# Optimization experiments

Hardware: AMD Instinct MI355X
Metric: run time of the kernel (lower is better)

The kernel has to match this reference:

```python
import jax, jax.numpy as jnp
import numpy as np

METRIC = (1.0, 1.0, 1.0, 1.0, -1.0)  # Cl(4,1) signature
N_HEADS = 8
EPS = 1e-6


def _cayley():
    # Cayley table C[a, b, k]: e_a * e_b = sum_k C[a,b,k] e_k, blades indexed by bitmask over 5 generators.
    C = np.zeros((32, 32, 32), dtype=np.float32)
    for a in range(32):
        for b in range(32):
            s = 0
            t = a >> 1
            while t:
                s += bin(t & b).count('1')
                t >>= 1
            sign = -1.0 if (s & 1) else 1.0
            for i in range(5):
                if (a & b) >> i & 1:
                    sign *= METRIC[i]
            C[a, b, a ^ b] = sign
    return C

_C_NP = _cayley()
GP_MAP = jnp.asarray(_C_NP)  # (32,32,32)
SIG = jnp.asarray(_C_NP[np.arange(32), np.arange(32), 0])  # blade square signs, (32,)


def normalize_cl41(x):
    # normalize each multivector (last-dim 32 blades) to unit RMS
    return x / jnp.sqrt(jnp.mean(x * x, axis=-1, keepdims=True) + EPS)


def versor_linear(x, W):
    # x: (B,S,I,32), W: (O,I,32); out_k = sum_{i,j,l} W[o,i,j] C[j,l,k] x[b,s,i,l]
    O, I, _ = W.shape
    W_op = jnp.einsum('oij,jlk->oilk', W, GP_MAP)  # (O,I,32,32)
    W_mat = W_op.transpose(1, 2, 0, 3).reshape(I * 32, O * 32)
    B, S = x.shape[0], x.shape[1]
    out = (x.reshape(B, S, I * 32) @ W_mat).reshape(B, S, O, 32)
    return normalize_cl41(out)


def versor_attention(x, Wq, Wk, Wv, Wo, lam):
    B, S, D, _ = x.shape
    H = N_HEADS
    hd = D // H

    def split_heads(t):  # (B,S,D,32) -> (B,H,S,hd,32)
        return t.reshape(B, S, H, hd, 32).transpose(0, 2, 1, 3, 4)

    q = split_heads(versor_linear(x, Wq))
    k = split_heads(versor_linear(x, Wk))
    v = split_heads(versor_linear(x, Wv))

    q_flat = (q * SIG).reshape(B, H, S, hd * 32)  # signature-weighted
    k_flat = k.reshape(B, H, S, hd * 32)

    scalar = jnp.einsum('bhsd,bhtd->bhst', q_flat, k_flat)
    scale = 1.0 / jnp.sqrt(jnp.asarray(hd, x.dtype))
    score = scalar * scale

    # torque term: sqrt(relu(|q|^2 |k|^2 - (q.k)^2) + eps) / sqrt(hd)
    q_norm_sq = jnp.sum(q_flat * q_flat, axis=-1)[..., :, None]  # (B,H,S,1)
    k_norm_sq = jnp.sum(k_flat * k_flat, axis=-1)[..., None, :]  # (B,H,1,S)
    torque = jnp.sqrt(jax.nn.relu(q_norm_sq * k_norm_sq - scalar * scalar) + EPS) * scale
    score = score + lam * torque

    probs = jax.nn.softmax(score, axis=-1)
    out = jnp.einsum('bhst,bhtdl->bhsdl', probs, v)  # (B,H,S,hd,32)
    out = out.transpose(0, 2, 1, 3, 4).reshape(B, S, D, 32)
    return versor_linear(out, Wo)


def setup_inputs() -> dict:
    key = jax.random.key(0)
    ks = jax.random.split(key, 5)
    B, S, D = 2, 1024, 128
    std = (2.0 / (D * 32)) ** 0.5  # Versor init
    x = jax.random.normal(ks[0], (B, S, D, 32), jnp.float32)
    Wq = jax.random.normal(ks[1], (D, D, 32), jnp.float32) * std
    Wk = jax.random.normal(ks[2], (D, D, 32), jnp.float32) * std
    Wv = jax.random.normal(ks[3], (D, D, 32), jnp.float32) * std
    Wo = jax.random.normal(ks[4], (D, D, 32), jnp.float32) * std
    attn_lambda = jnp.float32(0.1)
    return {'x': x, 'Wq': Wq, 'Wk': Wk, 'Wv': Wv, 'Wo': Wo, 'attn_lambda': attn_lambda}


def reference(x, Wq, Wk, Wv, Wo, attn_lambda):
    return versor_attention(x, Wq, Wk, Wv, Wo, attn_lambda)
```

## Files before the change

### kernel.cpp

```cpp
#include <hip/hip_runtime.h>
#include <stdint.h>

typedef __attribute__((ext_vector_type(4))) float    f32x4;
typedef __attribute__((ext_vector_type(8))) short    s16x8;
typedef __attribute__((ext_vector_type(4))) short    s16x4;
typedef __attribute__((ext_vector_type(8))) _Float16 f16x8;

#define DEV __device__ __forceinline__

DEV float blade_sign(int a, int b){
    int s = 0, t = a >> 1;
    while (t){ s += __popc(t & b); t >>= 1; }
    float sg = (s & 1) ? -1.0f : 1.0f;
    return ((a & b) & 16) ? -sg : sg;
}
DEV short f2h(float v){
    _Float16 h = (_Float16)v;
    return __builtin_bit_cast(short, h);
}
DEV float h2f(short b){
    return (float)__builtin_bit_cast(_Float16, b);
}
DEV void wait_vm(int n){
    if (n == 8)      asm volatile("s_waitcnt vmcnt(8)" ::: "memory");
    else if (n == 4) asm volatile("s_waitcnt vmcnt(4)" ::: "memory");
    else             asm volatile("s_waitcnt vmcnt(0)" ::: "memory");
}

__global__ __launch_bounds__(256) void cast_f32_f16(const float* __restrict__ in,
                                                    short* __restrict__ out){
    const size_t idx = (size_t)blockIdx.x * 256 + threadIdx.x;
    const float4* p = reinterpret_cast<const float4*>(in) + idx * 2;
    float4 a = p[0], b = p[1];
    s16x8 o;
    o[0]=f2h(a.x); o[1]=f2h(a.y); o[2]=f2h(a.z); o[3]=f2h(a.w);
    o[4]=f2h(b.x); o[5]=f2h(b.y); o[6]=f2h(b.z); o[7]=f2h(b.w);
    *reinterpret_cast<s16x8*>(out + idx * 8) = o;
}

DEV void build_wmat_body(const float* __restrict__ W, short* __restrict__ WmT,
                         int idx){
    const int n  = idx >> 9;
    const int kg = idx & 511;
    const int o = n >> 5, kb = n & 31;
    const int i = kg >> 2, l0 = (kg & 3) * 8;
    const float* wrow = W + (size_t)(o * 128 + i) * 32;
    s16x8 v;
    #pragma unroll
    for (int e = 0; e < 8; ++e){
        const int l = l0 + e, j = kb ^ l;
        v[e] = f2h(wrow[j] * blade_sign(j, l));
    }
    *reinterpret_cast<s16x8*>(WmT + (size_t)n * 4096 + kg * 8) = v;
}

__global__ __launch_bounds__(256) void build_wmat(const float* __restrict__ W,
                                                  short* __restrict__ WmT){
    build_wmat_body(W, WmT, blockIdx.x * 256 + threadIdx.x);
}

__global__ __launch_bounds__(256) void build_wmat3(const float* __restrict__ Wq,
                                                   const float* __restrict__ Wk,
                                                   const float* __restrict__ Wv,
                                                   short* __restrict__ WmT3){
    const int w = blockIdx.y;
    const float* W = (w == 0) ? Wq : ((w == 1) ? Wk : Wv);
    build_wmat_body(W, WmT3 + (size_t)w * 4096 * 4096,
                    blockIdx.x * 256 + threadIdx.x);
}

__global__ __launch_bounds__(256) void row_norms(const short* __restrict__ Q,
                                                 const short* __restrict__ Kq,
                                                 float* __restrict__ Nq,
                                                 float* __restrict__ Nk){
    const int row  = blockIdx.x * 4 + (threadIdx.x >> 6);
    const int lane = threadIdx.x & 63;
    const int b = row >> 13, h = (row >> 10) & 7, s = row & 1023;
    const size_t off = ((size_t)(b * 1024 + s)) * 4096 + h * 512 + lane * 8;
    s16x8 a = *reinterpret_cast<const s16x8*>(Q + off);
    s16x8 c = *reinterpret_cast<const s16x8*>(Kq + off);
    float sq = 0.f, sk = 0.f;
    #pragma unroll
    for (int e = 0; e < 8; ++e){
        float fa = h2f(a[e]); sq = fmaf(fa, fa, sq);
        float fc = h2f(c[e]); sk = fmaf(fc, fc, sk);
    }
    #pragma unroll
    for (int m = 1; m < 64; m <<= 1){
        sq += __shfl_xor(sq, m);
        sk += __shfl_xor(sk, m);
    }
    if (lane == 0){ Nq[row] = sq; Nk[row] = sk; }
}

__global__ __launch_bounds__(256) void softmax_rows(float* __restrict__ Sc){
    const int row  = blockIdx.x * 4 + (threadIdx.x >> 6);
    const int lane = threadIdx.x & 63;
    float* p = Sc + (size_t)row * 1024;
    float v[16];
    float mx = -3.0e38f;
    #pragma unroll
    for (int j = 0; j < 16; ++j){ v[j] = p[lane + j * 64]; mx = fmaxf(mx, v[j]); }
    #pragma unroll
    for (int m = 1; m < 64; m <<= 1) mx = fmaxf(mx, __shfl_xor(mx, m));
    float sum = 0.f;
    #pragma unroll
    for (int j = 0; j < 16; ++j){ v[j] = __expf(v[j] - mx); sum += v[j]; }
    #pragma unroll
    for (int m = 1; m < 64; m <<= 1) sum += __shfl_xor(sum, m);
    const float inv = 1.0f / sum;
    short* pb = reinterpret_cast<short*>(p);
    #pragma unroll
    for (int j = 0; j < 16; ++j) pb[lane + j * 64] = f2h(v[j] * inv);
}

#define GLOAD_LDS(gp, lp) \
    __builtin_amdgcn_global_load_lds( \
        (const __attribute__((address_space(1))) void*)(const void*)(gp), \
        (__attribute__((address_space(3))) void*)(void*)(lp), 16, 0, 0)

#define R3_TILE(T, WN, PF)                                                      \
  {                                                                             \
    const int bb = cur * 8192;                                                  \
    wait_vm(WN);                                                                \
    __builtin_amdgcn_s_barrier();                                               \
    asm volatile("" ::: "memory");                                              \
    __builtin_amdgcn_sched_barrier(0);                                          \
    const int sb = stg * 8192;                                                  \
    if (PF){                                                                    \
        GLOAD_LDS(gA0 + (size_t)((T) + 2) * 32, lds + sb + dA0);                \
        GLOAD_LDS(gA1 + (size_t)((T) + 2) * 32, lds + sb + dA1);                \
    }                                                                           \
    f16x8 av[4], bv[4];                                                         \
    _Pragma("unroll")                                                           \
    for (int i = 0; i < 4; ++i)                                                 \
        av[i] = *reinterpret_cast<const f16x8*>(lds + bb + ard + i * 512);      \
    bv[0] = *reinterpret_cast<const f16x8*>(lds + bb + brd + 0 * 512);          \
    bv[1] = *reinterpret_cast<const f16x8*>(lds + bb + brd + 1 * 512);          \
    __builtin_amdgcn_s_setprio(1);                                              \
    _Pragma("unroll")                                                           \
    for (int mi = 0; mi < 4; ++mi)                                              \
        _Pragma("unroll")                                                       \
        for (int ni = 0; ni < 2; ++ni)                                          \
            acc[mi][ni] = __builtin_amdgcn_mfma_f32_16x16x32_f16(               \
                av[mi], bv[ni], acc[mi][ni], 0, 0, 0);                          \
    __builtin_amdgcn_s_setprio(0);                                              \
    if (PF){                                                                    \
        GLOAD_LDS(gB0 + (size_t)((T) + 2) * 32, lds + sb + dB0);                \
        GLOAD_LDS(gB1 + (size_t)((T) + 2) * 32, lds + sb + dB1);                \
    }                                                                           \
    bv[2] = *reinterpret_cast<const f16x8*>(lds + bb + brd + 2 * 512);          \
    bv[3] = *reinterpret_cast<const f16x8*>(lds + bb + brd + 3 * 512);          \
    __builtin_amdgcn_s_setprio(1);                                              \
    _Pragma("unroll")                                                           \
    for (int mi = 0; mi < 4; ++mi)                                              \
        _Pragma("unroll")                                                       \
        for (int ni = 2; ni < 4; ++ni)                                          \
            acc[mi][ni] = __builtin_amdgcn_mfma_f32_16x16x32_f16(               \
                av[mi], bv[ni], acc[mi][ni], 0, 0, 0);                          \
    __builtin_amdgcn_s_setprio(0);                                              \
    cur = (cur == 2) ? 0 : cur + 1;                                             \
    stg = (stg == 2) ? 0 : stg + 1;                                             \
  }

template<int EPI, int CPX>
__global__ __launch_bounds__(256, 3) void versor_gemm_r3(
    const short* __restrict__ Abase, int lda,
    const short* __restrict__ Bbase, int ldb,
    int K, void* __restrict__ OutP,
    short* __restrict__ OQ, short* __restrict__ OK, short* __restrict__ OV)
{
    __shared__ short lds[3 * 8192];

    const int tid  = threadIdx.x;
    const int lane = tid & 63;
    const int wid  = tid >> 6;
    const int wr   = wid >> 1;
    const int wc   = wid & 1;
    const int z    = blockIdx.z;

    int bn, bm;
    if constexpr (CPX > 0){
        const int wg  = blockIdx.x + blockIdx.y * gridDim.x;
        const int xcd = wg & 7;
        const int u   = wg >> 3;
        bm = u & 15;
        bn = xcd * CPX + (u >> 4);
    } else {
        bn = blockIdx.x; bm = blockIdx.y;
    }

    const short* A = Abase;
    const short* B = Bbase;
    if constexpr (EPI == 5){
        A += (size_t)z * 1024 * 2048;
        B += (size_t)z * 512 * 1024;
    }
    const int row0 = bm * 128;
    const int col0 = bn * 128;

    const int jsw = ((lane & 3) ^ ((lane >> 3) & 3)) * 8;
    const short* gA0 = A + (size_t)(row0 + wid * 16 + (lane >> 2)) * lda + jsw;
    const short* gA1 = gA0 + (size_t)64 * lda;
    const short* gB0 = B + (size_t)(col0 + wid * 16 + (lane >> 2)) * ldb + jsw;
    const short* gB1 = gB0 + (size_t)64 * ldb;
    const int dA0 = wid * 512,        dA1 = 2048 + wid * 512;
    const int dB0 = 4096 + wid * 512, dB1 = 6144 + wid * 512;

    const int swz = ((lane >> 4) ^ (((lane & 15) >> 1) & 3)) * 8;
    const int ard = (wr * 64 + (lane & 15)) * 32 + swz;
    const int brd = 4096 + (wc * 64 + (lane & 15)) * 32 + swz;

    f32x4 acc[4][4];
    #pragma unroll
    for (int i = 0; i < 4; ++i)
        #pragma unroll
        for (int j = 0; j < 4; ++j)
            acc[i][j] = (f32x4){0.f, 0.f, 0.f, 0.f};

    const int NT = K >> 5;

    #pragma unroll
    for (int pt = 0; pt < 2; ++pt){
        const int sb = pt * 8192;
        GLOAD_LDS(gA0 + pt * 32, lds + sb + dA0);
        GLOAD_LDS(gA1 + pt * 32, lds + sb + dA1);
        GLOAD_LDS(gB0 + pt * 32, lds + sb + dB0);
        GLOAD_LDS(gB1 + pt * 32, lds + sb + dB1);
    }

    int cur = 0, stg = 2;
    for (int t = 0; t < NT - 1; ++t)
        R3_TILE(t, 4, (t + 2 < NT))
    R3_TILE(NT - 1, 0, false)

    const int rb = row0 + wr * 64 + (lane >> 4) * 4;
    const int cb = col0 + wc * 64 + (lane & 15);

    if constexpr (EPI == 0 || EPI == 3){
        #pragma unroll
        for (int mi = 0; mi < 4; ++mi){
            #pragma unroll
            for (int g = 0; g < 2; ++g){
                f32x4 a0 = acc[mi][2 * g], a1 = acc[mi][2 * g + 1];
                f32x4 ss = a0 * a0 + a1 * a1;
                #pragma unroll
                for (int m = 1; m < 16; m <<= 1){
                    ss.x += __shfl_xor(ss.x, m);
                    ss.y += __shfl_xor(ss.y, m);
                    ss.z += __shfl_xor(ss.z, m);
                    ss.w += __shfl_xor(ss.w, m);
                }
                f32x4 inv;
                inv.x = 1.0f / sqrtf(ss.x * 0.03125f + 1e-6f);
                inv.y = 1.0f / sqrtf(ss.y * 0.03125f + 1e-6f);
                inv.z = 1.0f / sqrtf(ss.z * 0.03125f + 1e-6f);
                inv.w = 1.0f / sqrtf(ss.w * 0.03125f + 1e-6f);
                acc[mi][2 * g]     = a0 * inv;
                acc[mi][2 * g + 1] = a1 * inv;
            }
        }
    }

    if constexpr (EPI == 0){
        const int zsel = col0 >> 12;
        const int cbm  = (col0 & 4095) + wc * 64 + (lane & 15);
        if (zsel == 0){
            const float sg0 = blade_sign(lane & 15, lane & 15);
            const float sg1 = blade_sign(16 | (lane & 15), 16 | (lane & 15));
            #pragma unroll
            for (int mi = 0; mi < 4; ++mi)
                #pragma unroll
                for (int ni = 0; ni < 4; ++ni){
                    const f32x4 v = acc[mi][ni] * ((ni & 1) ? sg1 : sg0);
                    #pragma unroll
                    for (int j = 0; j < 4; ++j)
                        OQ[(size_t)(rb + mi * 16 + j) * 4096 + (cbm + ni * 16)] = f2h(v[j]);
                }
        } else if (zsel == 1){
            #pragma unroll
            for (int mi = 0; mi < 4; ++mi)
                #pragma unroll
                for (int ni = 0; ni < 4; ++ni)
                    #pragma unroll
                    for (int j = 0; j < 4; ++j)
                        OK[(size_t)(rb + mi * 16 + j) * 4096 + (cbm + ni * 16)] = f2h(acc[mi][ni][j]);
        } else {
            #pragma unroll
            for (int mi = 0; mi < 4; ++mi){
                const int r = rb + mi * 16;
                const int b = r >> 10, tt = r & 1023;
                #pragma unroll
                for (int ni = 0; ni < 4; ++ni){
                    const int c = cbm + ni * 16;
                    const int h = c >> 9, f = c & 511;
                    s16x4 pv;
                    #pragma unroll
                    for (int j = 0; j < 4; ++j) pv[j] = f2h(acc[mi][ni][j]);
                    *reinterpret_cast<s16x4*>(OV + ((size_t)((b * 8 + h) * 512 + f)) * 1024 + tt) = pv;
                }
            }
        }
    }
    if constexpr (EPI == 3){
        float* Of = (float*)OutP;
        #pragma unroll
        for (int mi = 0; mi < 4; ++mi)
            #pragma unroll
            for (int ni = 0; ni < 4; ++ni)
                #pragma unroll
                for (int j = 0; j < 4; ++j)
                    Of[(size_t)(rb + mi * 16 + j) * 4096 + (cb + ni * 16)] = acc[mi][ni][j];
    }
    if constexpr (EPI == 5){
        short* Ob = (short*)OutP;
        const int b = z >> 3, h = z & 7;
        #pragma unroll
        for (int mi = 0; mi < 4; ++mi)
            #pragma unroll
            for (int ni = 0; ni < 4; ++ni)
                #pragma unroll
                for (int j = 0; j < 4; ++j)
                    Ob[(size_t)(b * 1024 + rb + mi * 16 + j) * 4096 + h * 512 + (cb + ni * 16)]
                        = f2h(acc[mi][ni][j]);
    }
}

#define SC_TILE(T, WN, PF)                                                      \
  {                                                                             \
    const int bb = ((T) & 3) * 16384;                                           \
    wait_vm(WN);                                                                \
    __builtin_amdgcn_s_barrier();                                               \
    asm volatile("" ::: "memory");                                              \
    __builtin_amdgcn_sched_barrier(0);                                          \
    if (PF){                                                                    \
        const int nb = (((T) + 3) & 3) * 16384;                                 \
        GLOAD_LDS(gA0 + (size_t)((T) + 3) * 32, lds + nb + dA0);                \
        GLOAD_LDS(gA1 + (size_t)((T) + 3) * 32, lds + nb + dA1);                \
    }                                                                           \
    f16x8 av[4], bv[4];                                                         \
    _Pragma("unroll")                                                           \
    for (int i = 0; i < 4; ++i){                                                \
        av[i] = *reinterpret_cast<const f16x8*>(lds + bb + ard + i * 512);      \
        bv[i] = *reinterpret_cast<const f16x8*>(lds + bb + brd + i * 512);      \
    }                                                                           \
    __builtin_amdgcn_s_setprio(1);                                              \
    _Pragma("unroll")                                                           \
    for (int mi = 0; mi < 4; ++mi)                                              \
        _Pragma("unroll")                                                       \
        for (int ni = 0; ni < 4; ++ni)                                          \
            acc[mi][ni] = __builtin_amdgcn_mfma_f32_16x16x32_f16(               \
                av[mi], bv[ni], acc[mi][ni], 0, 0, 0);                          \
    __builtin_amdgcn_s_setprio(0);                                              \
    if (PF){                                                                    \
        const int nb = (((T) + 3) & 3) * 16384;                                 \
        GLOAD_LDS(gB0 + (size_t)((T) + 3) * 32, lds + nb + dB0);                \
        GLOAD_LDS(gB1 + (size_t)((T) + 3) * 32, lds + nb + dB1);                \
    }                                                                           \
    f16x8 aw[4];                                                                \
    _Pragma("unroll")                                                           \
    for (int i = 0; i < 4; ++i)                                                 \
        aw[i] = *reinterpret_cast<const f16x8*>(lds + bb + ard + (4 + i) * 512);\
    __builtin_amdgcn_s_setprio(1);                                              \
    _Pragma("unroll")                                                           \
    for (int mi = 0; mi < 4; ++mi)                                              \
        _Pragma("unroll")                                                       \
        for (int ni = 0; ni < 4; ++ni)                                          \
            acc[4 + mi][ni] = __builtin_amdgcn_mfma_f32_16x16x32_f16(           \
                aw[mi], bv[ni], acc[4 + mi][ni], 0, 0, 0);                      \
    __builtin_amdgcn_s_setprio(0);                                              \
  }

__global__ __launch_bounds__(512, 2) void versor_gemm_sc(
    const short* __restrict__ Qbase, const short* __restrict__ Kbase,
    int K, float* __restrict__ OutP,
    const float* __restrict__ NqP, const float* __restrict__ NkP,
    const float* __restrict__ LamP)
{
    extern __shared__ short lds[];

    const int tid  = threadIdx.x;
    const int lane = tid & 63;
    const int wid  = tid >> 6;
    const int wm   = wid >> 2;
    const int wn   = wid & 3;
    const int z    = blockIdx.z;

    const int b = z >> 3, h = z & 7;
    const size_t off = (size_t)b * 1024 * 4096 + (size_t)h * 512;
    const short* A = Qbase + off;
    const short* B = Kbase + off;
    const int lda = 4096, ldb = 4096;
    const int row0 = blockIdx.y * 256;
    const int col0 = blockIdx.x * 256;

    const int jsw = ((lane & 3) ^ ((lane >> 3) & 3)) * 8;
    const short* gA0 = A + (size_t)(row0 + wid * 32 + (lane >> 2)) * lda + jsw;
    const short* gA1 = gA0 + (size_t)16 * lda;
    const short* gB0 = B + (size_t)(col0 + wid * 32 + (lane >> 2)) * ldb + jsw;
    const short* gB1 = gB0 + (size_t)16 * ldb;
    const int dA0 = wid * 1024, dA1 = dA0 + 512;
    const int dB0 = 8192 + wid * 1024, dB1 = dB0 + 512;

    const int swz = ((lane >> 4) ^ (((lane & 15) >> 1) & 3)) * 8;
    const int ard = (wm * 128 + (lane & 15)) * 32 + swz;
    const int brd = 8192 + (wn * 64 + (lane & 15)) * 32 + swz;

    f32x4 acc[8][4];
    #pragma unroll
    for (int i = 0; i < 8; ++i)
        #pragma unroll
        for (int j = 0; j < 4; ++j)
            acc[i][j] = (f32x4){0.f, 0.f, 0.f, 0.f};

    const int NT = K >> 5;

    #pragma unroll
    for (int pt = 0; pt < 3; ++pt){
        const int bb = pt * 16384;
        GLOAD_LDS(gA0 + pt * 32, lds + bb + dA0);
        GLOAD_LDS(gA1 + pt * 32, lds + bb + dA1);
        GLOAD_LDS(gB0 + pt * 32, lds + bb + dB0);
        GLOAD_LDS(gB1 + pt * 32, lds + bb + dB1);
    }

    for (int t = 0; t < NT - 2; ++t)
        SC_TILE(t, 8, (t + 3 < NT))
    SC_TILE(NT - 2, 4, false)
    SC_TILE(NT - 1, 0, false)

    const int rb = row0 + wm * 128 + (lane >> 4) * 4;
    const int cb = col0 + wn * 64 + (lane & 15);

    float* Of = OutP + (size_t)z * 1024 * 1024;
    const float lam = *LamP;
    const float* nq = NqP + z * 1024;
    const float* nk = NkP + z * 1024;
    #pragma unroll
    for (int mi = 0; mi < 8; ++mi)
        #pragma unroll
        for (int j = 0; j < 4; ++j){
            const int r = rb + mi * 16 + j;
            const float qn = nq[r];
            #pragma unroll
            for (int ni = 0; ni < 4; ++ni){
                const int c = cb + ni * 16;
                const float sc = acc[mi][ni][j];
                const float tq = sqrtf(fmaxf(qn * nk[c] - sc * sc, 0.0f) + 1e-6f);
                Of[(size_t)r * 1024 + c] = 0.25f * (sc + lam * tq);
            }
        }
}

extern "C" void kernel_launch(void* const* d_in, const int* in_sizes, int n_in,
                              void* d_out, int out_size, void* d_ws, size_t ws_size,
                              hipStream_t stream)
{
    (void)in_sizes; (void)n_in; (void)out_size; (void)ws_size;
    const float* x   = (const float*)d_in[0];
    const float* Wq  = (const float*)d_in[1];
    const float* Wk  = (const float*)d_in[2];
    const float* Wv  = (const float*)d_in[3];
    const float* Wo  = (const float*)d_in[4];
    const float* lam = (const float*)d_in[5];
    float* out = (float*)d_out;
    char*  ws  = (char*)d_ws;

    short* Xf   = (short*)(ws);
    short* WmT3 = (short*)(ws + (16u  << 20));
    short* Qf   = (short*)(ws + (112u << 20));
    short* Kf   = (short*)(ws + (128u << 20));
    short* Vt   = (short*)(ws + (144u << 20));
    float* Nq   = (float*)(ws + (160u << 20));
    float* Nk   = (float*)(ws + (160u << 20) + (64u << 10));
    float* Sc   = (float*)(ws + (16u  << 20));
    short* WmTo = (short*)(ws + (80u  << 20));
    short* Attn = Xf;

    const int DYN_LDS = 131072;
    hipFuncSetAttribute(reinterpret_cast<const void*>(versor_gemm_sc),
                        hipFuncAttributeMaxDynamicSharedMemorySize, DYN_LDS);

    dim3 blk(256), blk8(512);
    cast_f32_f16<<<4096, blk, 0, stream>>>(x, Xf);

    dim3 gw3(8192, 3);
    build_wmat3<<<gw3, blk, 0, stream>>>(Wq, Wk, Wv, WmT3);

    dim3 gqkv(96, 16, 1);
    versor_gemm_r3<0, 12><<<gqkv, blk, 0, stream>>>(
        Xf, 4096, WmT3, 4096, 4096, nullptr, Qf, Kf, Vt);

    row_norms<<<4096, blk, 0, stream>>>(Qf, Kf, Nq, Nk);

    build_wmat<<<8192, blk, 0, stream>>>(Wo, WmTo);

    dim3 gsc(4, 4, 16);
    versor_gemm_sc<<<gsc, blk8, DYN_LDS, stream>>>(Qf, Kf, 512, Sc, Nq, Nk, lam);
    softmax_rows<<<4096, blk, 0, stream>>>(Sc);

    dim3 gpv(4, 8, 16);
    versor_gemm_r3<5, 0><<<gpv, blk, 0, stream>>>(
        (const short*)Sc, 2048, Vt, 1024, 1024, Attn, nullptr, nullptr, nullptr);

    dim3 gfin(32, 16, 1);
    versor_gemm_r3<3, 4><<<gfin, blk, 0, stream>>>(
        Attn, 4096, WmTo, 4096, 4096, out, nullptr, nullptr, nullptr);
}
```

Measured before the change: 551.4 us.

## Add dedicated 256x128-tile QKV GEMM kernel with split prefetch scheduling

Replaces the generic r3 GEMM used for the fused QKV projection with a specialized kernel using 256x128 block tiles (each wave computing 128x64), a 3-stage LDS ring buffer, and B-tile prefetches interleaved between the two MFMA halves. The larger tile raises arithmetic intensity per LDS/global load and halves the grid. The normalization and Q/K/V scatter epilogue moves into the new kernel. The cost is more accumulator registers (128 floats) and 72KB LDS, which may limit occupancy to about 2 blocks per CU.

```diff
diff --git a/kernel.cpp b/kernel.cpp
--- a/kernel.cpp
+++ b/kernel.cpp
@@ -22,7 +22,9 @@
     return (float)__builtin_bit_cast(_Float16, b);
 }
 DEV void wait_vm(int n){
-    if (n == 8)      asm volatile("s_waitcnt vmcnt(8)" ::: "memory");
+    if (n == 12)     asm volatile("s_waitcnt vmcnt(12)" ::: "memory");
+    else if (n == 8) asm volatile("s_waitcnt vmcnt(8)" ::: "memory");
+    else if (n == 6) asm volatile("s_waitcnt vmcnt(6)" ::: "memory");
     else if (n == 4) asm volatile("s_waitcnt vmcnt(4)" ::: "memory");
     else             asm volatile("s_waitcnt vmcnt(0)" ::: "memory");
 }
@@ -119,6 +121,183 @@
         (const __attribute__((address_space(1))) void*)(const void*)(gp), \
         (__attribute__((address_space(3))) void*)(void*)(lp), 16, 0, 0)
 
+#define QKV_TILE(T, WN, PF)                                                     \
+  {                                                                             \
+    const int bb = cur * 12288;                                                 \
+    wait_vm(WN);                                                                \
+    __builtin_amdgcn_s_barrier();                                               \
+    asm volatile("" ::: "memory");                                              \
+    __builtin_amdgcn_sched_barrier(0);                                          \
+    const int sb = stg * 12288;                                                 \
+    if (PF){                                                                    \
+        GLOAD_LDS(gA0 + (size_t)((T) + 2) * 32, lds + sb + dA + 0 * 512);       \
+        GLOAD_LDS(gA1 + (size_t)((T) + 2) * 32, lds + sb + dA + 1 * 512);       \
+        GLOAD_LDS(gA2 + (size_t)((T) + 2) * 32, lds + sb + dA + 2 * 512);       \
+        GLOAD_LDS(gA3 + (size_t)((T) + 2) * 32, lds + sb + dA + 3 * 512);       \
+    }                                                                           \
+    f16x8 av[4], bv[4];                                                         \
+    _Pragma("unroll")                                                           \
+    for (int i = 0; i < 4; ++i){                                                \
+        av[i] = *reinterpret_cast<const f16x8*>(lds + bb + ard + i * 512);      \
+        bv[i] = *reinterpret_cast<const f16x8*>(lds + bb + brd + i * 512);      \
+    }                                                                           \
+    __builtin_amdgcn_s_setprio(1);                                              \
+    _Pragma("unroll")                                                           \
+    for (int mi = 0; mi < 4; ++mi)                                              \
+        _Pragma("unroll")                                                       \
+        for (int ni = 0; ni < 4; ++ni)                                          \
+            acc[mi][ni] = __builtin_amdgcn_mfma_f32_16x16x32_f16(               \
+                av[mi], bv[ni], acc[mi][ni], 0, 0, 0);                          \
+    __builtin_amdgcn_s_setprio(0);                                              \
+    if (PF){                                                                    \
+        GLOAD_LDS(gB0 + (size_t)((T) + 2) * 32, lds + sb + dB + 0 * 512);       \
+        GLOAD_LDS(gB1 + (size_t)((T) + 2) * 32, lds + sb + dB + 1 * 512);       \
+    }                                                                           \
+    f16x8 aw[4];                                                                \
+    _Pragma("unroll")                                                           \
+    for (int i = 0; i < 4; ++i)                                                 \
+        aw[i] = *reinterpret_cast<const f16x8*>(lds + bb + ard + (4 + i) * 512);\
+    __builtin_amdgcn_s_setprio(1);                                              \
+    _Pragma("unroll")                                                           \
+    for (int mi = 0; mi < 4; ++mi)                                              \
+        _Pragma("unroll")                                                       \
+        for (int ni = 0; ni < 4; ++ni)                                          \
+            acc[4 + mi][ni] = __builtin_amdgcn_mfma_f32_16x16x32_f16(           \
+                aw[mi], bv[ni], acc[4 + mi][ni], 0, 0, 0);                      \
+    __builtin_amdgcn_s_setprio(0);                                              \
+    cur = (cur == 2) ? 0 : cur + 1;                                             \
+    stg = (stg == 2) ? 0 : stg + 1;                                             \
+  }
+
+__global__ __launch_bounds__(256, 2) void versor_gemm_qkv2(
+    const short* __restrict__ Xf,
+    const short* __restrict__ WmT3,
+    short* __restrict__ OQ,
+    short* __restrict__ OK,
+    short* __restrict__ OV)
+{
+    extern __shared__ short lds[];
+
+    const int tid  = threadIdx.x;
+    const int lane = tid & 63;
+    const int wid  = tid >> 6;
+    const int wm   = wid >> 1;
+    const int wn   = wid & 1;
+
+    const int wg  = blockIdx.x + blockIdx.y * 96;
+    const int xcd = wg & 7;
+    const int u   = wg >> 3;
+    const int bm  = u & 7;
+    const int bn  = xcd * 12 + (u >> 3);
+    const int row0 = bm * 256;
+    const int col0 = bn * 128;
+
+    const int lda = 4096, ldb = 4096;
+
+    const int jsw = ((lane & 3) ^ ((lane >> 3) & 3)) * 8;
+    const short* gA0 = Xf + (size_t)(row0 + wid * 64 + (lane >> 2)) * lda + jsw;
+    const short* gA1 = gA0 + (size_t)16 * lda;
+    const short* gA2 = gA0 + (size_t)32 * lda;
+    const short* gA3 = gA0 + (size_t)48 * lda;
+    const short* gB0 = WmT3 + (size_t)(col0 + wid * 32 + (lane >> 2)) * ldb + jsw;
+    const short* gB1 = gB0 + (size_t)16 * ldb;
+    const int dA = wid * 4 * 512;
+    const int dB = 8192 + wid * 2 * 512;
+
+    const int swz = ((lane >> 4) ^ (((lane & 15) >> 1) & 3)) * 8;
+    const int ard = (wm * 128 + (lane & 15)) * 32 + swz;
+    const int brd = 8192 + (wn * 64 + (lane & 15)) * 32 + swz;
+
+    f32x4 acc[8][4];
+    #pragma unroll
+    for (int i = 0; i < 8; ++i)
+        #pragma unroll
+        for (int j = 0; j < 4; ++j)
+            acc[i][j] = (f32x4){0.f, 0.f, 0.f, 0.f};
+
+    const int NT = 4096 >> 5;
+
+    #pragma unroll
+    for (int pt = 0; pt < 2; ++pt){
+        const int sb = pt * 12288;
+        GLOAD_LDS(gA0 + pt * 32, lds + sb + dA + 0 * 512);
+        GLOAD_LDS(gA1 + pt * 32, lds + sb + dA + 1 * 512);
+        GLOAD_LDS(gA2 + pt * 32, lds + sb + dA + 2 * 512);
+        GLOAD_LDS(gA3 + pt * 32, lds + sb + dA + 3 * 512);
+        GLOAD_LDS(gB0 + pt * 32, lds + sb + dB + 0 * 512);
+        GLOAD_LDS(gB1 + pt * 32, lds + sb + dB + 1 * 512);
+    }
+
+    int cur = 0, stg = 2;
+    for (int t = 0; t < NT - 1; ++t)
+        QKV_TILE(t, 6, (t + 2 < NT))
+    QKV_TILE(NT - 1, 0, false)
+
+    const int rb = row0 + wm * 128 + (lane >> 4) * 4;
+
+    #pragma unroll
+    for (int mi = 0; mi < 8; ++mi){
+        #pragma unroll
+        for (int g = 0; g < 2; ++g){
+            f32x4 a0 = acc[mi][2 * g], a1 = acc[mi][2 * g + 1];
+            f32x4 ss = a0 * a0 + a1 * a1;
+            #pragma unroll
+            for (int m = 1; m < 16; m <<= 1){
+                ss.x += __shfl_xor(ss.x, m);
+                ss.y += __shfl_xor(ss.y, m);
+                ss.z += __shfl_xor(ss.z, m);
+                ss.w += __shfl_xor(ss.w, m);
+            }
+            f32x4 inv;
+            inv.x = 1.0f / sqrtf(ss.x * 0.03125f + 1e-6f);
+            inv.y = 1.0f / sqrtf(ss.y * 0.03125f + 1e-6f);
+            inv.z = 1.0f / sqrtf(ss.z * 0.03125f + 1e-6f);
+            inv.w = 1.0f / sqrtf(ss.w * 0.03125f + 1e-6f);
+            acc[mi][2 * g]     = a0 * inv;
+            acc[mi][2 * g + 1] = a1 * inv;
+        }
+    }
+
+    const int zsel = col0 >> 12;
+    const int cbm  = (col0 & 4095) + wn * 64 + (lane & 15);
+    if (zsel == 0){
+        const float sg0 = blade_sign(lane & 15, lane & 15);
+        const float sg1 = blade_sign(16 | (lane & 15), 16 | (lane & 15));
+        #pragma unroll
+        for (int mi = 0; mi < 8; ++mi)
+            #pragma unroll
+            for (int ni = 0; ni < 4; ++ni){
+                const f32x4 v = acc[mi][ni] * ((ni & 1) ? sg1 : sg0);
+                #pragma unroll
+                for (int j = 0; j < 4; ++j)
+                    OQ[(size_t)(rb + mi * 16 + j) * 4096 + (cbm + ni * 16)] = f2h(v[j]);
+            }
+    } else if (zsel == 1){
+        #pragma unroll
+        for (int mi = 0; mi < 8; ++mi)
+            #pragma unroll
+            for (int ni = 0; ni < 4; ++ni)
+                #pragma unroll
+                for (int j = 0; j < 4; ++j)
+                    OK[(size_t)(rb + mi * 16 + j) * 4096 + (cbm + ni * 16)] = f2h(acc[mi][ni][j]);
+    } else {
+        #pragma unroll
+        for (int mi = 0; mi < 8; ++mi){
+            const int r = rb + mi * 16;
+            const int b = r >> 10, tt = r & 1023;
+            #pragma unroll
+            for (int ni = 0; ni < 4; ++ni){
+                const int c = cbm + ni * 16;
+                const int h = c >> 9, f = c & 511;
+                s16x4 pv;
+                #pragma unroll
+                for (int j = 0; j < 4; ++j) pv[j] = f2h(acc[mi][ni][j]);
+                *reinterpret_cast<s16x4*>(OV + ((size_t)((b * 8 + h) * 512 + f)) * 1024 + tt) = pv;
+            }
+        }
+    }
+}
+
 #define R3_TILE(T, WN, PF)                                                      \
   {                                                                             \
     const int bb = cur * 8192;                                                  \
@@ -237,7 +416,7 @@
     const int rb = row0 + wr * 64 + (lane >> 4) * 4;
     const int cb = col0 + wc * 64 + (lane & 15);
 
-    if constexpr (EPI == 0 || EPI == 3){
+    if constexpr (EPI == 3){
         #pragma unroll
         for (int mi = 0; mi < 4; ++mi){
             #pragma unroll
@@ -260,49 +439,6 @@
                 acc[mi][2 * g + 1] = a1 * inv;
             }
         }
-    }
-
-    if constexpr (EPI == 0){
-        const int zsel = col0 >> 12;
-        const int cbm  = (col0 & 4095) + wc * 64 + (lane & 15);
-        if (zsel == 0){
-            const float sg0 = blade_sign(lane & 15, lane & 15);
-            const float sg1 = blade_sign(16 | (lane & 15), 16 | (lane & 15));
-            #pragma unroll
-            for (int mi = 0; mi < 4; ++mi)
-                #pragma unroll
-                for (int ni = 0; ni < 4; ++ni){
-                    const f32x4 v = acc[mi][ni] * ((ni & 1) ? sg1 : sg0);
-                    #pragma unroll
-                    for (int j = 0; j < 4; ++j)
-                        OQ[(size_t)(rb + mi * 16 + j) * 4096 + (cbm + ni * 16)] = f2h(v[j]);
-                }
-        } else if (zsel == 1){
-            #pragma unroll
-            for (int mi = 0; mi < 4; ++mi)
-                #pragma unroll
-                for (int ni = 0; ni < 4; ++ni)
-                    #pragma unroll
-                    for (int j = 0; j < 4; ++j)
-                        OK[(size_t)(rb + mi * 16 + j) * 4096 + (cbm + ni * 16)] = f2h(acc[mi][ni][j]);
-        } else {
-            #pragma unroll
-            for (int mi = 0; mi < 4; ++mi){
-                const int r = rb + mi * 16;
-                const int b = r >> 10, tt = r & 1023;
-                #pragma unroll
-                for (int ni = 0; ni < 4; ++ni){
-                    const int c = cbm + ni * 16;
-                    const int h = c >> 9, f = c & 511;
-                    s16x4 pv;
-                    #pragma unroll
-                    for (int j = 0; j < 4; ++j) pv[j] = f2h(acc[mi][ni][j]);
-                    *reinterpret_cast<s16x4*>(OV + ((size_t)((b * 8 + h) * 512 + f)) * 1024 + tt) = pv;
-                }
-            }
-        }
-    }
-    if constexpr (EPI == 3){
         float* Of = (float*)OutP;
         #pragma unroll
         for (int mi = 0; mi < 4; ++mi)
@@ -324,6 +460,7 @@
                     Ob[(size_t)(b * 1024 + rb + mi * 16 + j) * 4096 + h * 512 + (cb + ni * 16)]
                         = f2h(acc[mi][ni][j]);
     }
+    (void)OQ; (void)OK; (void)OV;
 }
 
 #define SC_TILE(T, WN, PF)                                                      \
@@ -477,9 +614,12 @@
     short* WmTo = (short*)(ws + (80u  << 20));
     short* Attn = Xf;
 
-    const int DYN_LDS = 131072;
+    const int SC_LDS  = 131072;
+    const int QKV_LDS = 73728;
     hipFuncSetAttribute(reinterpret_cast<const void*>(versor_gemm_sc),
-                        hipFuncAttributeMaxDynamicSharedMemorySize, DYN_LDS);
+                        hipFuncAttributeMaxDynamicSharedMemorySize, SC_LDS);
+    hipFuncSetAttribute(reinterpret_cast<const void*>(versor_gemm_qkv2),
+                        hipFuncAttributeMaxDynamicSharedMemorySize, QKV_LDS);
 
     dim3 blk(256), blk8(512);
     cast_f32_f16<<<4096, blk, 0, stream>>>(x, Xf);
@@ -487,16 +627,15 @@
     dim3 gw3(8192, 3);
     build_wmat3<<<gw3, blk, 0, stream>>>(Wq, Wk, Wv, WmT3);
 
-    dim3 gqkv(96, 16, 1);
-    versor_gemm_r3<0, 12><<<gqkv, blk, 0, stream>>>(
-        Xf, 4096, WmT3, 4096, 4096, nullptr, Qf, Kf, Vt);
+    dim3 gqkv(96, 8, 1);
+    versor_gemm_qkv2<<<gqkv, blk, QKV_LDS, stream>>>(Xf, WmT3, Qf, Kf, Vt);
 
     row_norms<<<4096, blk, 0, stream>>>(Qf, Kf, Nq, Nk);
 
     build_wmat<<<8192, blk, 0, stream>>>(Wo, WmTo);
 
     dim3 gsc(4, 4, 16);
-    versor_gemm_sc<<<gsc, blk8, DYN_LDS, stream>>>(Qf, Kf, 512, Sc, Nq, Nk, lam);
+    versor_gemm_sc<<<gsc, blk8, SC_LDS, stream>>>(Qf, Kf, 512, Sc, Nq, Nk, lam);
     softmax_rows<<<4096, blk, 0, stream>>>(Sc);
 
     dim3 gpv(4, 8, 16);
```

After: 525.7 us. 4.7% less time.
